# Performance work log

Hardware: AMD Instinct MI355X
Metric: run time of the kernel (lower is better)

## Reference

```python
import jax, jax.numpy as jnp
import numpy as np

MASK_VALUE = -1000000.0

def setup_inputs() -> dict:
    key = jax.random.key(0)
    ks = jax.random.split(key, 8)
    B, Lq, Lk = 8, 128, 512
    Dq = Dk = H = Dv = 256
    queries = jax.random.normal(ks[0], (B, Lq, Dq), dtype=jnp.float32)
    keys = jax.random.normal(ks[1], (B, Lk, Dk), dtype=jnp.float32)
    values = jax.random.normal(ks[2], (B, Lk, Dv), dtype=jnp.float32)
    valid_lens = jax.random.randint(ks[3], (B,), 1, Lk + 1).astype(jnp.int32)
    # Learned parameters (stored as (in, out) so x @ W matches torch Linear)
    Wq = jax.random.normal(ks[4], (Dq, H), dtype=jnp.float32) / np.sqrt(Dq)
    Wk = jax.random.normal(ks[5], (Dk, H), dtype=jnp.float32) / np.sqrt(Dk)
    wv = jax.random.normal(ks[6], (H,), dtype=jnp.float32) / np.sqrt(H)
    return {"queries": queries, "keys": keys, "values": values,
            "valid_lens": valid_lens, "Wq": Wq, "Wk": Wk, "wv": wv}

def reference(queries, keys, values, valid_lens, Wq, Wk, wv):
    # projections
    q = jnp.einsum('bqd,dh->bqh', queries, Wq)   # (B, Lq, H)
    k = jnp.einsum('bkd,dh->bkh', keys, Wk)      # (B, Lk, H)
    # additive score: tanh(q_i + k_j) . w_v  -> (B, Lq, Lk)
    features = jnp.tanh(q[:, :, None, :] + k[:, None, :, :])  # (B, Lq, Lk, H)
    scores = jnp.einsum('bqkh,h->bqk', features, wv)
    # masked softmax over k axis; masked positions set to -1e6 (as in torch src)
    Lk = keys.shape[1]
    mask = jnp.arange(Lk)[None, None, :] >= valid_lens[:, None, None]  # (B,1,Lk)
    scores = jnp.where(mask, MASK_VALUE, scores)
    attn = jax.nn.softmax(scores, axis=-1)
    # dropout p=0.0 -> identity
    return jnp.einsum('bqk,bkv->bqv', attn, values)  # (B, Lq, Dv)
```

## Files before the change

### kernel.cpp

```cpp
#include <hip/hip_runtime.h>
#include <hip/hip_bf16.h>


#define SCALE_2LOG2E 2.885390081777927f
#define LOG2E        1.4426950408889634f
#define NEG_BIG     -1.0e30f

__device__ __forceinline__ float fast_exp2(float x) {
#if __has_builtin(__builtin_amdgcn_exp2f)
    return __builtin_amdgcn_exp2f(x);
#else
    return exp2f(x);
#endif
}
__device__ __forceinline__ float fast_rcp(float x) {
#if __has_builtin(__builtin_amdgcn_rcpf)
    return __builtin_amdgcn_rcpf(x);
#else
    return __fdividef(1.0f, x);
#endif
}

__global__ __launch_bounds__(256) void proj_kernel(
    const float* __restrict__ queries, const float* __restrict__ keys,
    const float* __restrict__ Wq, const float* __restrict__ Wk,
    const int* __restrict__ valid_lens,
    float* __restrict__ qproj, float* __restrict__ kproj)
{
    const int mt = blockIdx.y, nt = blockIdx.x;
    const float* X; const float* W; float* P; int row0;
    if (mt < 16) { X = queries; W = Wq; P = qproj; row0 = mt * 64; }
    else {
        const int kr = mt * 64 - 1024;
        const int b = kr >> 9, loc = kr & 511;
        if (loc >= valid_lens[b]) return;
        X = keys; W = Wk; P = kproj; row0 = kr;
    }
    const int t  = threadIdx.x;
    const int tx = t & 15, ty = t >> 4;
    const int ar = t >> 2, ac = t & 3;
    const int br = t >> 4, bc = t & 15;
    const int n0 = nt * 64;

    __shared__ float as[16][68];
    __shared__ float bs[16][68];

    const float* Aptr = X + (size_t)(row0 + ar) * 256 + ac * 4;
    const float* Bptr = W + (size_t)br * 256 + n0 + bc * 4;

    float4 av = *(const float4*)Aptr;
    float4 bv = *(const float4*)Bptr;

    float acc[4][4];
#pragma unroll
    for (int i = 0; i < 4; ++i)
#pragma unroll
        for (int j = 0; j < 4; ++j) acc[i][j] = 0.f;

    for (int ch = 0; ch < 16; ++ch) {
        __syncthreads();
        as[ac * 4 + 0][ar] = av.x;
        as[ac * 4 + 1][ar] = av.y;
        as[ac * 4 + 2][ar] = av.z;
        as[ac * 4 + 3][ar] = av.w;
        *(float4*)&bs[br][bc * 4] = bv;
        __syncthreads();
        if (ch < 15) {
            av = *(const float4*)(Aptr + (ch + 1) * 16);
            bv = *(const float4*)(Bptr + (size_t)(ch + 1) * 16 * 256);
        }
#pragma unroll
        for (int kk = 0; kk < 16; ++kk) {
            const float4 af = *(const float4*)&as[kk][ty * 4];
            const float4 bf = *(const float4*)&bs[kk][tx * 4];
            acc[0][0] += af.x * bf.x; acc[0][1] += af.x * bf.y;
            acc[0][2] += af.x * bf.z; acc[0][3] += af.x * bf.w;
            acc[1][0] += af.y * bf.x; acc[1][1] += af.y * bf.y;
            acc[1][2] += af.y * bf.z; acc[1][3] += af.y * bf.w;
            acc[2][0] += af.z * bf.x; acc[2][1] += af.z * bf.y;
            acc[2][2] += af.z * bf.z; acc[2][3] += af.z * bf.w;
            acc[3][0] += af.w * bf.x; acc[3][1] += af.w * bf.y;
            acc[3][2] += af.w * bf.z; acc[3][3] += af.w * bf.w;
        }
    }
#pragma unroll
    for (int i = 0; i < 4; ++i) {
        float4 o;
        o.x = acc[i][0] * SCALE_2LOG2E; o.y = acc[i][1] * SCALE_2LOG2E;
        o.z = acc[i][2] * SCALE_2LOG2E; o.w = acc[i][3] * SCALE_2LOG2E;
        *(float4*)(P + (size_t)(row0 + ty * 4 + i) * 256 + n0 + tx * 4) = o;
    }
}

__global__ __launch_bounds__(256) void score_kernel(
    const float* __restrict__ qproj,
    const float* __restrict__ kproj,
    const float* __restrict__ wv,
    const int*   __restrict__ valid_lens,
    float* __restrict__ scores)
{
    const int b  = blockIdx.z;
    const int vlen = valid_lens[b];
    const int k0 = blockIdx.x * 16;
    if (k0 >= vlen) return;
    const int q0 = blockIdx.y * 16;
    const int t  = threadIdx.x;

    __shared__ float qs[16][260];
    __shared__ float ks[16][260];
    __shared__ float wl[256];

    {
        const float4* qsrc = (const float4*)(qproj + (size_t)(b * 128 + q0) * 256);
        const float4* ksrc = (const float4*)(kproj + ((size_t)b * 512 + k0) * 256);
        for (int i = t; i < 1024; i += 256) {
            *(float4*)&qs[i >> 6][(i & 63) * 4] = qsrc[i];
            *(float4*)&ks[i >> 6][(i & 63) * 4] = ksrc[i];
        }
        if (t < 64) *(float4*)&wl[t * 4] = ((const float4*)wv)[t];
    }
    __syncthreads();

    float wsum;
    {
        const float4 wq = *(const float4*)&wl[(t & 63) * 4];
        wsum = wq.x + wq.y + wq.z + wq.w;
#pragma unroll
        for (int o = 1; o < 64; o <<= 1) wsum += __shfl_xor(wsum, o);
    }

    const int tx = t & 15, ty = t >> 4;
    float acc = 0.f;
#pragma unroll 8
    for (int h0 = 0; h0 < 256; h0 += 4) {
        const float4 qf = *(const float4*)&qs[ty][h0];
        const float4 kf = *(const float4*)&ks[tx][h0];
        const float4 wf = *(const float4*)&wl[h0];
        acc += wf.x * fast_rcp(fast_exp2(qf.x + kf.x) + 1.f);
        acc += wf.y * fast_rcp(fast_exp2(qf.y + kf.y) + 1.f);
        acc += wf.z * fast_rcp(fast_exp2(qf.z + kf.z) + 1.f);
        acc += wf.w * fast_rcp(fast_exp2(qf.w + kf.w) + 1.f);
    }
    if (k0 + tx < vlen)
        scores[(size_t)(b * 128 + q0 + ty) * 512 + k0 + tx] = wsum - 2.f * acc;
}

__global__ __launch_bounds__(256) void softmax_pv_kernel(
    const float* __restrict__ scores,
    const float* __restrict__ values,
    const int*   __restrict__ valid_lens,
    float* __restrict__ out)
{
    __shared__ float attn[2][512];
    __shared__ float pout[2][256];
    const int b = blockIdx.y, q0 = blockIdx.x * 2;
    const int t = threadIdx.x, w = t >> 6, lane = t & 63;
    const int rr = w & 1, half = w >> 1, row = q0 + rr;
    const int vlen = valid_lens[b];

    const float* srow = scores + (size_t)(b * 128 + row) * 512;
    float sv[8];
#pragma unroll
    for (int j = 0; j < 8; ++j) {
        const int k = lane + 64 * j;
        sv[j] = (k < vlen) ? srow[k] : NEG_BIG;
    }

    float m = sv[0];
#pragma unroll
    for (int j = 1; j < 8; ++j) m = fmaxf(m, sv[j]);
#pragma unroll
    for (int o = 1; o < 64; o <<= 1) m = fmaxf(m, __shfl_xor(m, o));

    float sum = 0.f;
#pragma unroll
    for (int j = 0; j < 8; ++j) {
        sv[j] = fast_exp2((sv[j] - m) * LOG2E);
        sum += sv[j];
    }
#pragma unroll
    for (int o = 1; o < 64; o <<= 1) sum += __shfl_xor(sum, o);
    const float rs = fast_rcp(sum);

#pragma unroll
    for (int j = 0; j < 4; ++j) {
        const int jj = half * 4 + j;
        attn[rr][lane + 64 * jj] = sv[jj] * rs;
    }

    const int vl16 = (vlen + 15) & ~15;
    const int kbeg = half * 256;
    const int kend = min(vl16, kbeg + 256);
    const float* V = values + (size_t)b * 512 * 256 + lane * 4;

    float4 acc = {0.f, 0.f, 0.f, 0.f};
    for (int k0 = kbeg; k0 < kend; k0 += 16) {
#pragma unroll
        for (int g = 0; g < 4; ++g) {
            const int kk = k0 + g * 4;
            const float4 aq = *(const float4*)&attn[rr][kk];
            const float4 v0 = *(const float4*)(V + (size_t)(kk + 0) * 256);
            const float4 v1 = *(const float4*)(V + (size_t)(kk + 1) * 256);
            const float4 v2 = *(const float4*)(V + (size_t)(kk + 2) * 256);
            const float4 v3 = *(const float4*)(V + (size_t)(kk + 3) * 256);
            acc.x += aq.x * v0.x + aq.y * v1.x + aq.z * v2.x + aq.w * v3.x;
            acc.y += aq.x * v0.y + aq.y * v1.y + aq.z * v2.y + aq.w * v3.y;
            acc.z += aq.x * v0.z + aq.y * v1.z + aq.z * v2.z + aq.w * v3.z;
            acc.w += aq.x * v0.w + aq.y * v1.w + aq.z * v2.w + aq.w * v3.w;
        }
    }

    if (half) *(float4*)&pout[rr][lane * 4] = acc;
    __syncthreads();
    if (!half) {
        const float4 p = *(const float4*)&pout[rr][lane * 4];
        acc.x += p.x; acc.y += p.y; acc.z += p.z; acc.w += p.w;
        *(float4*)(out + (size_t)(b * 128 + row) * 256 + lane * 4) = acc;
    }
}

extern "C" void kernel_launch(void* const* d_in, const int* in_sizes, int n_in,
                              void* d_out, int out_size, void* d_ws, size_t ws_size,
                              hipStream_t stream) {
    const float* queries = (const float*)d_in[0];
    const float* keys    = (const float*)d_in[1];
    const float* values  = (const float*)d_in[2];
    const int*   vlens   = (const int*)  d_in[3];
    const float* Wq      = (const float*)d_in[4];
    const float* Wk      = (const float*)d_in[5];
    const float* wv      = (const float*)d_in[6];
    float* out = (float*)d_out;

    float* qproj  = (float*)d_ws;
    float* kproj  = qproj + 1024 * 256;
    float* scores = kproj + 4096 * 256;

    proj_kernel<<<dim3(4, 80), 256, 0, stream>>>(queries, keys, Wq, Wk,
                                                 vlens, qproj, kproj);
    score_kernel<<<dim3(32, 8, 8), 256, 0, stream>>>(qproj, kproj, wv,
                                                     vlens, scores);
    softmax_pv_kernel<<<dim3(64, 8), 256, 0, stream>>>(scores, values,
                                                       vlens, out);
}
```

Before: 141.5 us.

## Double-buffer projection GEMM, register-block score tiles, share V loads across rows

The projection GEMM now uses double-buffered shared-memory tiles with a K-chunk of 32, so there is one barrier per chunk instead of two. The score kernel processes 32 keys per block, and each thread computes a 2x2 (query, key) tile over half of the hidden dimension, then combines the halves with a shuffle. This reuses the q and k shared-memory loads across four tanh evaluations and halves the grid. The softmax-PV kernel splits the key range across four waves, each computing both query rows, so every V load feeds two rows; the partial sums are reduced through shared memory. The cost is more registers and a larger key-block padding for small valid lengths.

```diff
diff --git a/kernel.cpp b/kernel.cpp
--- a/kernel.cpp
+++ b/kernel.cpp
@@ -32,24 +32,37 @@
     if (mt < 16) { X = queries; W = Wq; P = qproj; row0 = mt * 64; }
     else {
         const int kr = mt * 64 - 1024;
-        const int b = kr >> 9, loc = kr & 511;
-        if (loc >= valid_lens[b]) return;
+        const int bb = kr >> 9, loc = kr & 511;
+        if (loc >= valid_lens[bb]) return;
         X = keys; W = Wk; P = kproj; row0 = kr;
     }
     const int t  = threadIdx.x;
     const int tx = t & 15, ty = t >> 4;
     const int ar = t >> 2, ac = t & 3;
-    const int br = t >> 4, bc = t & 15;
+    const int br = t >> 3, bc = t & 7;
     const int n0 = nt * 64;
 
-    __shared__ float as[16][68];
-    __shared__ float bs[16][68];
+    __shared__ float as[2][32][68];
+    __shared__ float bs[2][32][68];
 
     const float* Aptr = X + (size_t)(row0 + ar) * 256 + ac * 4;
     const float* Bptr = W + (size_t)br * 256 + n0 + bc * 4;
 
-    float4 av = *(const float4*)Aptr;
-    float4 bv = *(const float4*)Bptr;
+    float4 av0 = *(const float4*)(Aptr);
+    float4 av1 = *(const float4*)(Aptr + 16);
+    float4 bv0 = *(const float4*)(Bptr);
+    float4 bv1 = *(const float4*)(Bptr + 32);
+    as[0][ac * 4 + 0][ar] = av0.x;  as[0][ac * 4 + 1][ar] = av0.y;
+    as[0][ac * 4 + 2][ar] = av0.z;  as[0][ac * 4 + 3][ar] = av0.w;
+    as[0][ac * 4 + 16][ar] = av1.x; as[0][ac * 4 + 17][ar] = av1.y;
+    as[0][ac * 4 + 18][ar] = av1.z; as[0][ac * 4 + 19][ar] = av1.w;
+    *(float4*)&bs[0][br][bc * 4]      = bv0;
+    *(float4*)&bs[0][br][bc * 4 + 32] = bv1;
+    av0 = *(const float4*)(Aptr + 32);
+    av1 = *(const float4*)(Aptr + 48);
+    bv0 = *(const float4*)(Bptr + 32 * 256);
+    bv1 = *(const float4*)(Bptr + 32 * 256 + 32);
+    __syncthreads();
 
     float acc[4][4];
 #pragma unroll
@@ -57,22 +70,26 @@
 #pragma unroll
         for (int j = 0; j < 4; ++j) acc[i][j] = 0.f;
 
-    for (int ch = 0; ch < 16; ++ch) {
-        __syncthreads();
-        as[ac * 4 + 0][ar] = av.x;
-        as[ac * 4 + 1][ar] = av.y;
-        as[ac * 4 + 2][ar] = av.z;
-        as[ac * 4 + 3][ar] = av.w;
-        *(float4*)&bs[br][bc * 4] = bv;
-        __syncthreads();
-        if (ch < 15) {
-            av = *(const float4*)(Aptr + (ch + 1) * 16);
-            bv = *(const float4*)(Bptr + (size_t)(ch + 1) * 16 * 256);
+    for (int ch = 0; ch < 8; ++ch) {
+        const int cur = ch & 1, nxt = cur ^ 1;
+        if (ch < 7) {
+            as[nxt][ac * 4 + 0][ar] = av0.x;  as[nxt][ac * 4 + 1][ar] = av0.y;
+            as[nxt][ac * 4 + 2][ar] = av0.z;  as[nxt][ac * 4 + 3][ar] = av0.w;
+            as[nxt][ac * 4 + 16][ar] = av1.x; as[nxt][ac * 4 + 17][ar] = av1.y;
+            as[nxt][ac * 4 + 18][ar] = av1.z; as[nxt][ac * 4 + 19][ar] = av1.w;
+            *(float4*)&bs[nxt][br][bc * 4]      = bv0;
+            *(float4*)&bs[nxt][br][bc * 4 + 32] = bv1;
         }
-#pragma unroll
-        for (int kk = 0; kk < 16; ++kk) {
-            const float4 af = *(const float4*)&as[kk][ty * 4];
-            const float4 bf = *(const float4*)&bs[kk][tx * 4];
+        if (ch < 6) {
+            av0 = *(const float4*)(Aptr + (ch + 2) * 32);
+            av1 = *(const float4*)(Aptr + (ch + 2) * 32 + 16);
+            bv0 = *(const float4*)(Bptr + (size_t)(ch + 2) * 32 * 256);
+            bv1 = *(const float4*)(Bptr + (size_t)(ch + 2) * 32 * 256 + 32);
+        }
+#pragma unroll
+        for (int kk = 0; kk < 32; ++kk) {
+            const float4 af = *(const float4*)&as[cur][kk][ty * 4];
+            const float4 bf = *(const float4*)&bs[cur][kk][tx * 4];
             acc[0][0] += af.x * bf.x; acc[0][1] += af.x * bf.y;
             acc[0][2] += af.x * bf.z; acc[0][3] += af.x * bf.w;
             acc[1][0] += af.y * bf.x; acc[1][1] += af.y * bf.y;
@@ -82,6 +99,7 @@
             acc[3][0] += af.w * bf.x; acc[3][1] += af.w * bf.y;
             acc[3][2] += af.w * bf.z; acc[3][3] += af.w * bf.w;
         }
+        __syncthreads();
     }
 #pragma unroll
     for (int i = 0; i < 4; ++i) {
@@ -101,22 +119,22 @@
 {
     const int b  = blockIdx.z;
     const int vlen = valid_lens[b];
-    const int k0 = blockIdx.x * 16;
+    const int k0 = blockIdx.x * 32;
     if (k0 >= vlen) return;
     const int q0 = blockIdx.y * 16;
     const int t  = threadIdx.x;
 
     __shared__ float qs[16][260];
-    __shared__ float ks[16][260];
+    __shared__ float ks[32][260];
     __shared__ float wl[256];
 
     {
         const float4* qsrc = (const float4*)(qproj + (size_t)(b * 128 + q0) * 256);
+        for (int i = t; i < 1024; i += 256)
+            *(float4*)&qs[i >> 6][(i & 63) * 4] = qsrc[i];
         const float4* ksrc = (const float4*)(kproj + ((size_t)b * 512 + k0) * 256);
-        for (int i = t; i < 1024; i += 256) {
-            *(float4*)&qs[i >> 6][(i & 63) * 4] = qsrc[i];
+        for (int i = t; i < 2048; i += 256)
             *(float4*)&ks[i >> 6][(i & 63) * 4] = ksrc[i];
-        }
         if (t < 64) *(float4*)&wl[t * 4] = ((const float4*)wv)[t];
     }
     __syncthreads();
@@ -129,20 +147,46 @@
         for (int o = 1; o < 64; o <<= 1) wsum += __shfl_xor(wsum, o);
     }
 
-    const int tx = t & 15, ty = t >> 4;
-    float acc = 0.f;
+    const int hg = t & 1, kp = (t >> 1) & 15, qp = t >> 5;
+    const int hb = hg * 128;
+    float a00 = 0.f, a01 = 0.f, a10 = 0.f, a11 = 0.f;
 #pragma unroll 8
-    for (int h0 = 0; h0 < 256; h0 += 4) {
-        const float4 qf = *(const float4*)&qs[ty][h0];
-        const float4 kf = *(const float4*)&ks[tx][h0];
-        const float4 wf = *(const float4*)&wl[h0];
-        acc += wf.x * fast_rcp(fast_exp2(qf.x + kf.x) + 1.f);
-        acc += wf.y * fast_rcp(fast_exp2(qf.y + kf.y) + 1.f);
-        acc += wf.z * fast_rcp(fast_exp2(qf.z + kf.z) + 1.f);
-        acc += wf.w * fast_rcp(fast_exp2(qf.w + kf.w) + 1.f);
-    }
-    if (k0 + tx < vlen)
-        scores[(size_t)(b * 128 + q0 + ty) * 512 + k0 + tx] = wsum - 2.f * acc;
+    for (int hh = 0; hh < 32; ++hh) {
+        const int h = hb + hh * 4;
+        const float4 qa = *(const float4*)&qs[qp][h];
+        const float4 qb = *(const float4*)&qs[qp + 8][h];
+        const float4 ka = *(const float4*)&ks[kp][h];
+        const float4 kb = *(const float4*)&ks[kp + 16][h];
+        const float4 wf = *(const float4*)&wl[h];
+        a00 += wf.x * fast_rcp(fast_exp2(qa.x + ka.x) + 1.f);
+        a01 += wf.x * fast_rcp(fast_exp2(qa.x + kb.x) + 1.f);
+        a10 += wf.x * fast_rcp(fast_exp2(qb.x + ka.x) + 1.f);
+        a11 += wf.x * fast_rcp(fast_exp2(qb.x + kb.x) + 1.f);
+        a00 += wf.y * fast_rcp(fast_exp2(qa.y + ka.y) + 1.f);
+        a01 += wf.y * fast_rcp(fast_exp2(qa.y + kb.y) + 1.f);
+        a10 += wf.y * fast_rcp(fast_exp2(qb.y + ka.y) + 1.f);
+        a11 += wf.y * fast_rcp(fast_exp2(qb.y + kb.y) + 1.f);
+        a00 += wf.z * fast_rcp(fast_exp2(qa.z + ka.z) + 1.f);
+        a01 += wf.z * fast_rcp(fast_exp2(qa.z + kb.z) + 1.f);
+        a10 += wf.z * fast_rcp(fast_exp2(qb.z + ka.z) + 1.f);
+        a11 += wf.z * fast_rcp(fast_exp2(qb.z + kb.z) + 1.f);
+        a00 += wf.w * fast_rcp(fast_exp2(qa.w + ka.w) + 1.f);
+        a01 += wf.w * fast_rcp(fast_exp2(qa.w + kb.w) + 1.f);
+        a10 += wf.w * fast_rcp(fast_exp2(qb.w + ka.w) + 1.f);
+        a11 += wf.w * fast_rcp(fast_exp2(qb.w + kb.w) + 1.f);
+    }
+    a00 += __shfl_xor(a00, 1);
+    a01 += __shfl_xor(a01, 1);
+    a10 += __shfl_xor(a10, 1);
+    a11 += __shfl_xor(a11, 1);
+
+    if (hg == 0) {
+        float* r0 = scores + (size_t)(b * 128 + q0 + qp) * 512;
+        float* r1 = r0 + 8 * 512;
+        const int c0 = k0 + kp, c1 = k0 + kp + 16;
+        if (c0 < vlen) { r0[c0] = wsum - 2.f * a00; r1[c0] = wsum - 2.f * a10; }
+        if (c1 < vlen) { r0[c1] = wsum - 2.f * a01; r1[c1] = wsum - 2.f * a11; }
+    }
 }
 
 __global__ __launch_bounds__(256) void softmax_pv_kernel(
@@ -152,70 +196,99 @@
     float* __restrict__ out)
 {
     __shared__ float attn[2][512];
-    __shared__ float pout[2][256];
+    __shared__ float4 pout[4][2][64];
     const int b = blockIdx.y, q0 = blockIdx.x * 2;
     const int t = threadIdx.x, w = t >> 6, lane = t & 63;
-    const int rr = w & 1, half = w >> 1, row = q0 + rr;
     const int vlen = valid_lens[b];
 
-    const float* srow = scores + (size_t)(b * 128 + row) * 512;
-    float sv[8];
+    const float* s0 = scores + (size_t)(b * 128 + q0) * 512;
+    const float* s1 = s0 + 512;
+    float sv0[8], sv1[8];
 #pragma unroll
     for (int j = 0; j < 8; ++j) {
         const int k = lane + 64 * j;
-        sv[j] = (k < vlen) ? srow[k] : NEG_BIG;
-    }
-
-    float m = sv[0];
-#pragma unroll
-    for (int j = 1; j < 8; ++j) m = fmaxf(m, sv[j]);
-#pragma unroll
-    for (int o = 1; o < 64; o <<= 1) m = fmaxf(m, __shfl_xor(m, o));
-
-    float sum = 0.f;
+        const bool ok = k < vlen;
+        sv0[j] = ok ? s0[k] : NEG_BIG;
+        sv1[j] = ok ? s1[k] : NEG_BIG;
+    }
+
+    float m0 = sv0[0], m1 = sv1[0];
+#pragma unroll
+    for (int j = 1; j < 8; ++j) { m0 = fmaxf(m0, sv0[j]); m1 = fmaxf(m1, sv1[j]); }
+#pragma unroll
+    for (int o = 1; o < 64; o <<= 1) {
+        m0 = fmaxf(m0, __shfl_xor(m0, o));
+        m1 = fmaxf(m1, __shfl_xor(m1, o));
+    }
+    float su0 = 0.f, su1 = 0.f;
 #pragma unroll
     for (int j = 0; j < 8; ++j) {
-        sv[j] = fast_exp2((sv[j] - m) * LOG2E);
-        sum += sv[j];
-    }
-#pragma unroll
-    for (int o = 1; o < 64; o <<= 1) sum += __shfl_xor(sum, o);
-    const float rs = fast_rcp(sum);
-
-#pragma unroll
-    for (int j = 0; j < 4; ++j) {
-        const int jj = half * 4 + j;
-        attn[rr][lane + 64 * jj] = sv[jj] * rs;
-    }
-
-    const int vl16 = (vlen + 15) & ~15;
-    const int kbeg = half * 256;
-    const int kend = min(vl16, kbeg + 256);
+        sv0[j] = fast_exp2((sv0[j] - m0) * LOG2E); su0 += sv0[j];
+        sv1[j] = fast_exp2((sv1[j] - m1) * LOG2E); su1 += sv1[j];
+    }
+#pragma unroll
+    for (int o = 1; o < 64; o <<= 1) {
+        su0 += __shfl_xor(su0, o);
+        su1 += __shfl_xor(su1, o);
+    }
+    const float rs0 = fast_rcp(su0), rs1 = fast_rcp(su1);
+
+#pragma unroll
+    for (int j = 0; j < 8; ++j) {
+        attn[0][lane + 64 * j] = sv0[j] * rs0;
+        attn[1][lane + 64 * j] = sv1[j] * rs1;
+    }
+
+    const int kq = w * 128;
+    const int kend = min(kq + 128, (vlen + 7) & ~7);
     const float* V = values + (size_t)b * 512 * 256 + lane * 4;
-
-    float4 acc = {0.f, 0.f, 0.f, 0.f};
-    for (int k0 = kbeg; k0 < kend; k0 += 16) {
-#pragma unroll
-        for (int g = 0; g < 4; ++g) {
-            const int kk = k0 + g * 4;
-            const float4 aq = *(const float4*)&attn[rr][kk];
-            const float4 v0 = *(const float4*)(V + (size_t)(kk + 0) * 256);
-            const float4 v1 = *(const float4*)(V + (size_t)(kk + 1) * 256);
-            const float4 v2 = *(const float4*)(V + (size_t)(kk + 2) * 256);
-            const float4 v3 = *(const float4*)(V + (size_t)(kk + 3) * 256);
-            acc.x += aq.x * v0.x + aq.y * v1.x + aq.z * v2.x + aq.w * v3.x;
-            acc.y += aq.x * v0.y + aq.y * v1.y + aq.z * v2.y + aq.w * v3.y;
-            acc.z += aq.x * v0.z + aq.y * v1.z + aq.z * v2.z + aq.w * v3.z;
-            acc.w += aq.x * v0.w + aq.y * v1.w + aq.z * v2.w + aq.w * v3.w;
-        }
-    }
-
-    if (half) *(float4*)&pout[rr][lane * 4] = acc;
+    float4 acc0 = {0.f, 0.f, 0.f, 0.f};
+    float4 acc1 = {0.f, 0.f, 0.f, 0.f};
+
+    for (int k = kq; k < kend; k += 8) {
+        const float* Vp = V + (size_t)k * 256;
+        const float4 v0 = *(const float4*)(Vp + 0 * 256);
+        const float4 v1 = *(const float4*)(Vp + 1 * 256);
+        const float4 v2 = *(const float4*)(Vp + 2 * 256);
+        const float4 v3 = *(const float4*)(Vp + 3 * 256);
+        const float4 v4 = *(const float4*)(Vp + 4 * 256);
+        const float4 v5 = *(const float4*)(Vp + 5 * 256);
+        const float4 v6 = *(const float4*)(Vp + 6 * 256);
+        const float4 v7 = *(const float4*)(Vp + 7 * 256);
+        const float4 a0 = *(const float4*)&attn[0][k];
+        const float4 a4 = *(const float4*)&attn[0][k + 4];
+        const float4 b0 = *(const float4*)&attn[1][k];
+        const float4 b4 = *(const float4*)&attn[1][k + 4];
+        acc0.x += a0.x*v0.x + a0.y*v1.x + a0.z*v2.x + a0.w*v3.x;
+        acc0.y += a0.x*v0.y + a0.y*v1.y + a0.z*v2.y + a0.w*v3.y;
+        acc0.z += a0.x*v0.z + a0.y*v1.z + a0.z*v2.z + a0.w*v3.z;
+        acc0.w += a0.x*v0.w + a0.y*v1.w + a0.z*v2.w + a0.w*v3.w;
+        acc1.x += b0.x*v0.x + b0.y*v1.x + b0.z*v2.x + b0.w*v3.x;
+        acc1.y += b0.x*v0.y + b0.y*v1.y + b0.z*v2.y + b0.w*v3.y;
+        acc1.z += b0.x*v0.z + b0.y*v1.z + b0.z*v2.z + b0.w*v3.z;
+        acc1.w += b0.x*v0.w + b0.y*v1.w + b0.z*v2.w + b0.w*v3.w;
+        acc0.x += a4.x*v4.x + a4.y*v5.x + a4.z*v6.x + a4.w*v7.x;
+        acc0.y += a4.x*v4.y + a4.y*v5.y + a4.z*v6.y + a4.w*v7.y;
+        acc0.z += a4.x*v4.z + a4.y*v5.z + a4.z*v6.z + a4.w*v7.z;
+        acc0.w += a4.x*v4.w + a4.y*v5.w + a4.z*v6.w + a4.w*v7.w;
+        acc1.x += b4.x*v4.x + b4.y*v5.x + b4.z*v6.x + b4.w*v7.x;
+        acc1.y += b4.x*v4.y + b4.y*v5.y + b4.z*v6.y + b4.w*v7.y;
+        acc1.z += b4.x*v4.z + b4.y*v5.z + b4.z*v6.z + b4.w*v7.z;
+        acc1.w += b4.x*v4.w + b4.y*v5.w + b4.z*v6.w + b4.w*v7.w;
+    }
+
+    pout[w][0][lane] = acc0;
+    pout[w][1][lane] = acc1;
     __syncthreads();
-    if (!half) {
-        const float4 p = *(const float4*)&pout[rr][lane * 4];
-        acc.x += p.x; acc.y += p.y; acc.z += p.z; acc.w += p.w;
-        *(float4*)(out + (size_t)(b * 128 + row) * 256 + lane * 4) = acc;
+    if (t < 128) {
+        const int r = t >> 6, lid = t & 63;
+        float4 s = pout[0][r][lid];
+        const float4 p1 = pout[1][r][lid], p2 = pout[2][r][lid], p3 = pout[3][r][lid];
+        s.x += p1.x + p2.x + p3.x;
+        s.y += p1.y + p2.y + p3.y;
+        s.z += p1.z + p2.z + p3.z;
+        s.w += p1.w + p2.w + p3.w;
+        *(float4*)(out + (size_t)(b * 128 + q0 + r) * 256 + lid * 4) = s;
     }
 }
 
@@ -237,7 +310,7 @@
 
     proj_kernel<<<dim3(4, 80), 256, 0, stream>>>(queries, keys, Wq, Wk,
                                                  vlens, qproj, kproj);
-    score_kernel<<<dim3(32, 8, 8), 256, 0, stream>>>(qproj, kproj, wv,
+    score_kernel<<<dim3(16, 8, 8), 256, 0, stream>>>(qproj, kproj, wv,
                                                      vlens, scores);
     softmax_pv_kernel<<<dim3(64, 8), 256, 0, stream>>>(scores, values,
                                                        vlens, out);
```

New measurement: 128.2 us. 9.4% less time.
